# Performance work log

Hardware: AMD Instinct MI355X
Metric: run time of the kernel (lower is better)

## Reference

```python
import jax, jax.numpy as jnp
import numpy as np

N_NODES = 100000
N_EDGES = 1600000
F_IN, F_HID, N_CLS = 128, 128, 16


def setup_inputs() -> dict:
    key = jax.random.key(0)
    ks = jax.random.split(key, 6)
    x = jax.random.normal(ks[0], (N_NODES, F_IN), dtype=jnp.float32)
    edge_index = jax.random.randint(ks[1], (2, N_EDGES), 0, N_NODES, dtype=jnp.int64)
    # Glorot-ish scaled weights (PyG GCNConv uses glorot init, bias zeros)
    W1 = jax.random.normal(ks[2], (F_IN, F_HID), dtype=jnp.float32) * (1.0 / np.sqrt(F_IN))
    b1 = jnp.zeros((F_HID,), dtype=jnp.float32)
    W2 = jax.random.normal(ks[3], (F_HID, N_CLS), dtype=jnp.float32) * (1.0 / np.sqrt(F_HID))
    b2 = jnp.zeros((N_CLS,), dtype=jnp.float32)
    return {"x": x, "edge_index": edge_index, "W1": W1, "b1": b1, "W2": W2, "b2": b2}


def _gcn_conv(x, src, dst, W, b, num_nodes):
    """PyG GCNConv: y = D^{-1/2} (A + I) D^{-1/2} (x W) + b.
    src/dst already include self-loops."""
    h = x @ W  # [N, F_out]
    deg = jax.ops.segment_sum(jnp.ones_like(dst, dtype=h.dtype), dst, num_segments=num_nodes)
    dis = jnp.where(deg > 0, jax.lax.rsqrt(jnp.maximum(deg, 1e-12)), 0.0)
    norm = dis[src] * dis[dst]  # [E+N]
    msg = h[src] * norm[:, None]  # gather + scale  [E+N, F_out]
    out = jax.ops.segment_sum(msg, dst, num_segments=num_nodes)  # scatter-add at targets
    return out + b


def reference(x, edge_index, W1, b1, W2, b2):
    num_nodes = x.shape[0]
    loops = jnp.arange(num_nodes, dtype=edge_index.dtype)
    src = jnp.concatenate([edge_index[0], loops])
    dst = jnp.concatenate([edge_index[1], loops])
    h = _gcn_conv(x, src, dst, W1, b1, num_nodes)
    h = jax.nn.relu(h)
    # F.dropout with training=False (eval mode) is identity
    h = _gcn_conv(h, src, dst, W2, b2, num_nodes)
    return jax.nn.log_softmax(h, axis=1)
```

## Files before the change

### kernel.cpp

```cpp
#include <hip/hip_runtime.h>
#include <math.h>

#define N_NODES 100000
#define N_EDGES 1600000
#define NBINS 391
#define NCHUNK 400
#define CHUNK 4000
#define M_H (NBINS * NCHUNK)
#define NBLK_H 611

typedef __attribute__((ext_vector_type(8))) short bf16x8;
typedef __attribute__((ext_vector_type(4))) float f32x4;
typedef __attribute__((ext_vector_type(2))) float f32x2;

__device__ __forceinline__ unsigned short f2bf(float f) {
    unsigned int u = __float_as_uint(f);
    u += 0x7FFF + ((u >> 16) & 1);
    return (unsigned short)(u >> 16);
}
__device__ __forceinline__ float bf_lo(unsigned int u) { return __uint_as_float(u << 16); }
__device__ __forceinline__ float bf_hi(unsigned int u) { return __uint_as_float(u & 0xFFFF0000u); }
__device__ __forceinline__ f32x2 bfpair(unsigned int u) {
    f32x2 r; r.x = bf_lo(u); r.y = bf_hi(u); return r;
}


__global__ __launch_bounds__(256) void passA_kernel(const int* __restrict__ dst,
                                                    int* __restrict__ H) {
    __shared__ int lh[NBINS];
    int tid = threadIdx.x, c = blockIdx.x;
    for (int i = tid; i < NBINS; i += 256) lh[i] = 0;
    __syncthreads();
    int base = c * CHUNK;
    #pragma unroll
    for (int i = 0; i < 16; ++i) {
        int o = i * 256 + tid;
        if (o < CHUNK) atomicAdd(&lh[dst[base + o] >> 8], 1);
    }
    __syncthreads();
    for (int i = tid; i < NBINS; i += 256) H[i * NCHUNK + c] = lh[i];
}

__global__ __launch_bounds__(256) void scanB1_kernel(int* __restrict__ H,
                                                     int* __restrict__ blk2) {
    __shared__ int s[256];
    int t = threadIdx.x, i = blockIdx.x * 256 + t;
    int v = (i < M_H) ? H[i] : 0;
    s[t] = v;
    __syncthreads();
    for (int off = 1; off < 256; off <<= 1) {
        int u = (t >= off) ? s[t - off] : 0;
        __syncthreads();
        s[t] += u;
        __syncthreads();
    }
    if (i < M_H) H[i] = s[t] - v;
    if (t == 255) blk2[blockIdx.x] = s[255];
}

__global__ __launch_bounds__(1024) void scanB2_kernel(int* __restrict__ blk2) {
    __shared__ int s[1024];
    int t = threadIdx.x;
    int v = (t < NBLK_H) ? blk2[t] : 0;
    s[t] = v;
    __syncthreads();
    for (int off = 1; off < 1024; off <<= 1) {
        int u = (t >= off) ? s[t - off] : 0;
        __syncthreads();
        s[t] += u;
        __syncthreads();
    }
    if (t < NBLK_H) blk2[t] = s[t] - v;
}

__global__ __launch_bounds__(256) void passC_kernel(const int* __restrict__ src,
                                                    const int* __restrict__ dst,
                                                    const int* __restrict__ H,
                                                    const int* __restrict__ blk2,
                                                    int* __restrict__ rec,
                                                    const float* __restrict__ x,
                                                    const float* __restrict__ W1,
                                                    const float* __restrict__ W2,
                                                    ushort* __restrict__ xb,
                                                    ushort* __restrict__ W1T,
                                                    ushort* __restrict__ W2T) {
    int b = blockIdx.x;
    if (b < NCHUNK) {
        __shared__ int base[NBINS];
        __shared__ int rk[NBINS];
        int tid = threadIdx.x;
        for (int i = tid; i < NBINS; i += 256) {
            int idx = i * NCHUNK + b;
            base[i] = H[idx] + blk2[idx >> 8];
            rk[i] = 0;
        }
        __syncthreads();
        int estart = b * CHUNK;
        #pragma unroll
        for (int i = 0; i < 16; ++i) {
            int o = i * 256 + tid;
            if (o < CHUNK) {
                int e = estart + o;
                int d = dst[e];
                int bin = d >> 8;
                int r = atomicAdd(&rk[bin], 1);
                rec[base[bin] + r] = src[e] | ((d & 255) << 17);
            }
        }
    } else if (b < NCHUNK + 12500) {
        int i = (b - NCHUNK) * 256 + threadIdx.x;
        float4 v = *(const float4*)&x[i * 4];
        ushort4 o;
        o.x = f2bf(v.x); o.y = f2bf(v.y); o.z = f2bf(v.z); o.w = f2bf(v.w);
        *(ushort4*)&xb[i * 4] = o;
    } else {
        int j = (b - NCHUNK - 12500) * 256 + threadIdx.x;
        if (j < 16384) {
            int k = j >> 7, n = j & 127;
            W1T[n * 128 + k] = f2bf(W1[j]);
        } else {
            int q = j - 16384;
            int k = q >> 4, n = q & 15;
            W2T[n * 128 + k] = f2bf(W2[q]);
        }
    }
}

__global__ __launch_bounds__(256) void passD_kernel(const int* __restrict__ H,
                                                    const int* __restrict__ blk2,
                                                    const int* __restrict__ rec,
                                                    int* __restrict__ col,
                                                    int* __restrict__ cnt,
                                                    float* __restrict__ dis) {
    __shared__ int fh[256];
    __shared__ int s[256];
    __shared__ int run[256];
    int b = blockIdx.x, t = threadIdx.x;
    int i0 = b * NCHUNK;
    int estart = H[i0] + blk2[i0 >> 8];
    int eend;
    if (b == NBINS - 1) eend = N_EDGES;
    else { int i1 = (b + 1) * NCHUNK; eend = H[i1] + blk2[i1 >> 8]; }
    fh[t] = 0;
    __syncthreads();
    for (int e = estart + t; e < eend; e += 256)
        atomicAdd(&fh[rec[e] >> 17], 1);
    __syncthreads();
    int v = fh[t];
    s[t] = v;
    __syncthreads();
    for (int off = 1; off < 256; off <<= 1) {
        int u = (t >= off) ? s[t - off] : 0;
        __syncthreads();
        s[t] += u;
        __syncthreads();
    }
    int node = b * 256 + t;
    int start = estart + s[t] - v;
    run[t] = start;
    if (node < N_NODES) {
        cnt[node] = start;
        dis[node] = rsqrtf((float)v + 1.0f);
    }
    __syncthreads();
    for (int e = estart + t; e < eend; e += 256) {
        int r = rec[e];
        int p = atomicAdd(&run[r >> 17], 1);
        col[p] = r & 0x1FFFF;
    }
}


__global__ __launch_bounds__(256) void gather1_kernel(const int* __restrict__ col,
                                                      const int* __restrict__ cnt,
                                                      const float* __restrict__ dis,
                                                      const unsigned int* __restrict__ xb,
                                                      unsigned int* __restrict__ xa) {
    int t = threadIdx.x;
    int node = blockIdx.x * 4 + (t >> 6);
    int lane = t & 63;
    float dn = dis[node];
    int beg = cnt[node];
    int end = (node == N_NODES - 1) ? N_EDGES : cnt[node + 1];
    unsigned int su = xb[node * 64 + lane];
    f32x2 a0 = bfpair(su) * dn;
    f32x2 a1 = {0.f, 0.f}, a2 = {0.f, 0.f}, a3 = {0.f, 0.f};
    f32x2 a4 = {0.f, 0.f}, a5 = {0.f, 0.f}, a6 = {0.f, 0.f}, a7 = {0.f, 0.f};
    int k = beg;
    for (; k + 8 <= end; k += 8) {
        int s0 = col[k], s1 = col[k + 1], s2 = col[k + 2], s3 = col[k + 3];
        int s4 = col[k + 4], s5 = col[k + 5], s6 = col[k + 6], s7 = col[k + 7];
        float w0 = dis[s0], w1 = dis[s1], w2 = dis[s2], w3 = dis[s3];
        float w4 = dis[s4], w5 = dis[s5], w6 = dis[s6], w7 = dis[s7];
        unsigned int u0 = xb[s0 * 64 + lane], u1 = xb[s1 * 64 + lane];
        unsigned int u2 = xb[s2 * 64 + lane], u3 = xb[s3 * 64 + lane];
        unsigned int u4 = xb[s4 * 64 + lane], u5 = xb[s5 * 64 + lane];
        unsigned int u6 = xb[s6 * 64 + lane], u7 = xb[s7 * 64 + lane];
        a0 += bfpair(u0) * w0;
        a1 += bfpair(u1) * w1;
        a2 += bfpair(u2) * w2;
        a3 += bfpair(u3) * w3;
        a4 += bfpair(u4) * w4;
        a5 += bfpair(u5) * w5;
        a6 += bfpair(u6) * w6;
        a7 += bfpair(u7) * w7;
    }
    for (; k + 4 <= end; k += 4) {
        int s0 = col[k], s1 = col[k + 1], s2 = col[k + 2], s3 = col[k + 3];
        float w0 = dis[s0], w1 = dis[s1], w2 = dis[s2], w3 = dis[s3];
        unsigned int u0 = xb[s0 * 64 + lane], u1 = xb[s1 * 64 + lane];
        unsigned int u2 = xb[s2 * 64 + lane], u3 = xb[s3 * 64 + lane];
        a0 += bfpair(u0) * w0;
        a1 += bfpair(u1) * w1;
        a2 += bfpair(u2) * w2;
        a3 += bfpair(u3) * w3;
    }
    for (; k < end; ++k) {
        int s = col[k];
        float w = dis[s];
        a0 += bfpair(xb[s * 64 + lane]) * w;
    }
    f32x2 r = (((a0 + a1) + (a2 + a3)) + ((a4 + a5) + (a6 + a7))) * dn;
    xa[node * 64 + lane] = (unsigned int)f2bf(r.x) | ((unsigned int)f2bf(r.y) << 16);
}


__global__ __launch_bounds__(256) void mlp_kernel(const ushort* __restrict__ xa,
                                                  const ushort* __restrict__ W1T,
                                                  const float* __restrict__ b1,
                                                  const ushort* __restrict__ W2T,
                                                  ushort* __restrict__ h2b) {
    __shared__ ushort sh[4][16][136];
    int t = threadIdx.x;
    int wave = t >> 6, lane = t & 63;
    int l = lane & 15, quad = lane >> 4;
    int m0 = blockIdx.x * 64 + wave * 16;
    bool valid = (m0 < N_NODES);
    int row = valid ? (m0 + l) : 0;

    f32x4 acc[8] = {};
    #pragma unroll
    for (int kk = 0; kk < 4; ++kk) {
        bf16x8 a = *(const bf16x8*)&xa[row * 128 + kk * 32 + quad * 8];
        #pragma unroll
        for (int nt = 0; nt < 8; ++nt) {
            bf16x8 b = *(const bf16x8*)&W1T[(nt * 16 + l) * 128 + kk * 32 + quad * 8];
            acc[nt] = __builtin_amdgcn_mfma_f32_16x16x32_bf16(a, b, acc[nt], 0, 0, 0);
        }
    }
    #pragma unroll
    for (int nt = 0; nt < 8; ++nt) {
        float bias = b1[nt * 16 + l];
        #pragma unroll
        for (int r = 0; r < 4; ++r)
            sh[wave][quad * 4 + r][nt * 16 + l] = f2bf(fmaxf(acc[nt][r] + bias, 0.0f));
    }
    __syncthreads();

    f32x4 acc2 = {};
    #pragma unroll
    for (int kk = 0; kk < 4; ++kk) {
        bf16x8 a2 = *(const bf16x8*)&sh[wave][l][kk * 32 + quad * 8];
        bf16x8 bw = *(const bf16x8*)&W2T[l * 128 + kk * 32 + quad * 8];
        acc2 = __builtin_amdgcn_mfma_f32_16x16x32_bf16(a2, bw, acc2, 0, 0, 0);
    }
    if (valid) {
        #pragma unroll
        for (int r = 0; r < 4; ++r)
            h2b[(m0 + quad * 4 + r) * 16 + l] = f2bf(acc2[r]);
    }
}


__global__ __launch_bounds__(256) void gather2_lsm_kernel(const int* __restrict__ col,
                                                          const int* __restrict__ cnt,
                                                          const float* __restrict__ dis,
                                                          const unsigned int* __restrict__ h2p,
                                                          const float* __restrict__ b2,
                                                          float* __restrict__ out) {
    int t = threadIdx.x;
    int node = blockIdx.x * 32 + (t >> 3);
    int c = t & 7;
    float dn = dis[node];
    int beg = cnt[node];
    int end = (node == N_NODES - 1) ? N_EDGES : cnt[node + 1];
    unsigned int su = h2p[node * 8 + c];
    f32x2 a0 = bfpair(su) * dn;
    f32x2 a1 = {0.f, 0.f}, a2 = {0.f, 0.f}, a3 = {0.f, 0.f};
    f32x2 a4 = {0.f, 0.f}, a5 = {0.f, 0.f}, a6 = {0.f, 0.f}, a7 = {0.f, 0.f};
    int k = beg;
    for (; k + 8 <= end; k += 8) {
        int s0 = col[k], s1 = col[k + 1], s2 = col[k + 2], s3 = col[k + 3];
        int s4 = col[k + 4], s5 = col[k + 5], s6 = col[k + 6], s7 = col[k + 7];
        float w0 = dis[s0], w1 = dis[s1], w2 = dis[s2], w3 = dis[s3];
        float w4 = dis[s4], w5 = dis[s5], w6 = dis[s6], w7 = dis[s7];
        unsigned int u0 = h2p[s0 * 8 + c], u1 = h2p[s1 * 8 + c];
        unsigned int u2 = h2p[s2 * 8 + c], u3 = h2p[s3 * 8 + c];
        unsigned int u4 = h2p[s4 * 8 + c], u5 = h2p[s5 * 8 + c];
        unsigned int u6 = h2p[s6 * 8 + c], u7 = h2p[s7 * 8 + c];
        a0 += bfpair(u0) * w0;
        a1 += bfpair(u1) * w1;
        a2 += bfpair(u2) * w2;
        a3 += bfpair(u3) * w3;
        a4 += bfpair(u4) * w4;
        a5 += bfpair(u5) * w5;
        a6 += bfpair(u6) * w6;
        a7 += bfpair(u7) * w7;
    }
    for (; k + 4 <= end; k += 4) {
        int s0 = col[k], s1 = col[k + 1], s2 = col[k + 2], s3 = col[k + 3];
        float w0 = dis[s0], w1 = dis[s1], w2 = dis[s2], w3 = dis[s3];
        unsigned int u0 = h2p[s0 * 8 + c], u1 = h2p[s1 * 8 + c];
        unsigned int u2 = h2p[s2 * 8 + c], u3 = h2p[s3 * 8 + c];
        a0 += bfpair(u0) * w0;
        a1 += bfpair(u1) * w1;
        a2 += bfpair(u2) * w2;
        a3 += bfpair(u3) * w3;
    }
    for (; k < end; ++k) {
        int s = col[k];
        float w = dis[s];
        a0 += bfpair(h2p[s * 8 + c]) * w;
    }
    f32x2 r = ((a0 + a1) + (a2 + a3)) + ((a4 + a5) + (a6 + a7));
    float2 bb = ((const float2*)b2)[c];
    float v0 = r.x * dn + bb.x;
    float v1 = r.y * dn + bb.y;
    float m = fmaxf(v0, v1);
    #pragma unroll
    for (int off = 1; off < 8; off <<= 1) m = fmaxf(m, __shfl_xor(m, off, 8));
    float ssum = expf(v0 - m) + expf(v1 - m);
    #pragma unroll
    for (int off = 1; off < 8; off <<= 1) ssum += __shfl_xor(ssum, off, 8);
    float lg = m + logf(ssum);
    ((float2*)out)[node * 8 + c] = make_float2(v0 - lg, v1 - lg);
}


extern "C" void kernel_launch(void* const* d_in, const int* in_sizes, int n_in,
                              void* d_out, int out_size, void* d_ws, size_t ws_size,
                              hipStream_t stream) {
    const float* x  = (const float*)d_in[0];
    const int*   ei = (const int*)d_in[1];
    const float* W1 = (const float*)d_in[2];
    const float* b1 = (const float*)d_in[3];
    const float* W2 = (const float*)d_in[4];
    const float* b2 = (const float*)d_in[5];
    float* out = (float*)d_out;

    const int* src = ei;
    const int* dst = ei + N_EDGES;

    char* ws = (char*)d_ws;
    ushort* xb   = (ushort*)(ws + 0);
    ushort* h2b  = (ushort*)(ws + 0);
    ushort* xa   = (ushort*)(ws + 25600000);
    int*    rec  = (int*)   (ws + 25600000);
    int*    H    = (int*)   (ws + 32000000);
    int*    col  = (int*)   (ws + 51200000);
    float*  dis  = (float*) (ws + 57600000);
    int*    cnt  = (int*)   (ws + 58000000);
    int*    blk2 = (int*)   (ws + 58400000);
    ushort* W1T  = (ushort*)(ws + 58404096);
    ushort* W2T  = (ushort*)(ws + 58436864);

    passA_kernel      <<<NCHUNK, 256, 0, stream>>>(dst, H);
    scanB1_kernel     <<<NBLK_H, 256, 0, stream>>>(H, blk2);
    scanB2_kernel     <<<1, 1024, 0, stream>>>(blk2);
    passC_kernel      <<<NCHUNK + 12500 + 72, 256, 0, stream>>>(src, dst, H, blk2, rec,
                                                                x, W1, W2, xb, W1T, W2T);
    passD_kernel      <<<NBINS, 256, 0, stream>>>(H, blk2, rec, col, cnt, dis);

    gather1_kernel    <<<N_NODES / 4, 256, 0, stream>>>(col, cnt, dis,
                                                        (const unsigned int*)xb,
                                                        (unsigned int*)xa);
    mlp_kernel        <<<1563, 256, 0, stream>>>(xa, W1T, b1, W2T, h2b);
    gather2_lsm_kernel<<<3125, 256, 0, stream>>>(col, cnt, dis,
                                                 (const unsigned int*)h2b, b2, out);
}
```

Baseline: 272.7 us.

## Fuse first-layer neighbor gather into the MLP kernel via shared memory

Merges the layer-1 aggregation kernel into the MLP kernel. Each wave gathers 16 nodes sequentially into a shared-memory tile, and the MFMA matmuls then read that tile instead of a global intermediate. This removes the global write and re-read of the aggregated feature buffer and one kernel launch. The workspace layout changes so h2b no longer aliases xb. The cost is fewer, larger blocks with more LDS per block. That likely lowers resident waves and memory-level parallelism for the latency-bound gather, and adds serial per-wave node loops with tail imbalance.

```diff
diff --git a/kernel.cpp b/kernel.cpp
--- a/kernel.cpp
+++ b/kernel.cpp
@@ -171,77 +171,77 @@
 }
 
 
-__global__ __launch_bounds__(256) void gather1_kernel(const int* __restrict__ col,
-                                                      const int* __restrict__ cnt,
-                                                      const float* __restrict__ dis,
-                                                      const unsigned int* __restrict__ xb,
-                                                      unsigned int* __restrict__ xa) {
-    int t = threadIdx.x;
-    int node = blockIdx.x * 4 + (t >> 6);
-    int lane = t & 63;
-    float dn = dis[node];
-    int beg = cnt[node];
-    int end = (node == N_NODES - 1) ? N_EDGES : cnt[node + 1];
-    unsigned int su = xb[node * 64 + lane];
-    f32x2 a0 = bfpair(su) * dn;
-    f32x2 a1 = {0.f, 0.f}, a2 = {0.f, 0.f}, a3 = {0.f, 0.f};
-    f32x2 a4 = {0.f, 0.f}, a5 = {0.f, 0.f}, a6 = {0.f, 0.f}, a7 = {0.f, 0.f};
-    int k = beg;
-    for (; k + 8 <= end; k += 8) {
-        int s0 = col[k], s1 = col[k + 1], s2 = col[k + 2], s3 = col[k + 3];
-        int s4 = col[k + 4], s5 = col[k + 5], s6 = col[k + 6], s7 = col[k + 7];
-        float w0 = dis[s0], w1 = dis[s1], w2 = dis[s2], w3 = dis[s3];
-        float w4 = dis[s4], w5 = dis[s5], w6 = dis[s6], w7 = dis[s7];
-        unsigned int u0 = xb[s0 * 64 + lane], u1 = xb[s1 * 64 + lane];
-        unsigned int u2 = xb[s2 * 64 + lane], u3 = xb[s3 * 64 + lane];
-        unsigned int u4 = xb[s4 * 64 + lane], u5 = xb[s5 * 64 + lane];
-        unsigned int u6 = xb[s6 * 64 + lane], u7 = xb[s7 * 64 + lane];
-        a0 += bfpair(u0) * w0;
-        a1 += bfpair(u1) * w1;
-        a2 += bfpair(u2) * w2;
-        a3 += bfpair(u3) * w3;
-        a4 += bfpair(u4) * w4;
-        a5 += bfpair(u5) * w5;
-        a6 += bfpair(u6) * w6;
-        a7 += bfpair(u7) * w7;
-    }
-    for (; k + 4 <= end; k += 4) {
-        int s0 = col[k], s1 = col[k + 1], s2 = col[k + 2], s3 = col[k + 3];
-        float w0 = dis[s0], w1 = dis[s1], w2 = dis[s2], w3 = dis[s3];
-        unsigned int u0 = xb[s0 * 64 + lane], u1 = xb[s1 * 64 + lane];
-        unsigned int u2 = xb[s2 * 64 + lane], u3 = xb[s3 * 64 + lane];
-        a0 += bfpair(u0) * w0;
-        a1 += bfpair(u1) * w1;
-        a2 += bfpair(u2) * w2;
-        a3 += bfpair(u3) * w3;
-    }
-    for (; k < end; ++k) {
-        int s = col[k];
-        float w = dis[s];
-        a0 += bfpair(xb[s * 64 + lane]) * w;
-    }
-    f32x2 r = (((a0 + a1) + (a2 + a3)) + ((a4 + a5) + (a6 + a7))) * dn;
-    xa[node * 64 + lane] = (unsigned int)f2bf(r.x) | ((unsigned int)f2bf(r.y) << 16);
-}
-
-
-__global__ __launch_bounds__(256) void mlp_kernel(const ushort* __restrict__ xa,
-                                                  const ushort* __restrict__ W1T,
-                                                  const float* __restrict__ b1,
-                                                  const ushort* __restrict__ W2T,
-                                                  ushort* __restrict__ h2b) {
-    __shared__ ushort sh[4][16][136];
+__global__ __launch_bounds__(256) void gather_mlp_kernel(const int* __restrict__ col,
+                                                         const int* __restrict__ cnt,
+                                                         const float* __restrict__ dis,
+                                                         const unsigned int* __restrict__ xb,
+                                                         const ushort* __restrict__ W1T,
+                                                         const float* __restrict__ b1,
+                                                         const ushort* __restrict__ W2T,
+                                                         ushort* __restrict__ h2b) {
+    __shared__ ushort shx[64][136];
+    __shared__ ushort shh[4][16][136];
     int t = threadIdx.x;
     int wave = t >> 6, lane = t & 63;
     int l = lane & 15, quad = lane >> 4;
-    int m0 = blockIdx.x * 64 + wave * 16;
-    bool valid = (m0 < N_NODES);
-    int row = valid ? (m0 + l) : 0;
+    int m0 = blockIdx.x * 64;
+
+    for (int i = 0; i < 16; ++i) {
+        int node = m0 + wave * 16 + i;
+        unsigned int packed = 0;
+        if (node < N_NODES) {
+            float dn = dis[node];
+            int beg = cnt[node];
+            int end = (node == N_NODES - 1) ? N_EDGES : cnt[node + 1];
+            unsigned int su = xb[node * 64 + lane];
+            f32x2 a0 = bfpair(su) * dn;
+            f32x2 a1 = {0.f, 0.f}, a2 = {0.f, 0.f}, a3 = {0.f, 0.f};
+            f32x2 a4 = {0.f, 0.f}, a5 = {0.f, 0.f}, a6 = {0.f, 0.f}, a7 = {0.f, 0.f};
+            int k = beg;
+            for (; k + 8 <= end; k += 8) {
+                int s0 = col[k], s1 = col[k + 1], s2 = col[k + 2], s3 = col[k + 3];
+                int s4 = col[k + 4], s5 = col[k + 5], s6 = col[k + 6], s7 = col[k + 7];
+                float w0 = dis[s0], w1 = dis[s1], w2 = dis[s2], w3 = dis[s3];
+                float w4 = dis[s4], w5 = dis[s5], w6 = dis[s6], w7 = dis[s7];
+                unsigned int u0 = xb[s0 * 64 + lane], u1 = xb[s1 * 64 + lane];
+                unsigned int u2 = xb[s2 * 64 + lane], u3 = xb[s3 * 64 + lane];
+                unsigned int u4 = xb[s4 * 64 + lane], u5 = xb[s5 * 64 + lane];
+                unsigned int u6 = xb[s6 * 64 + lane], u7 = xb[s7 * 64 + lane];
+                a0 += bfpair(u0) * w0;
+                a1 += bfpair(u1) * w1;
+                a2 += bfpair(u2) * w2;
+                a3 += bfpair(u3) * w3;
+                a4 += bfpair(u4) * w4;
+                a5 += bfpair(u5) * w5;
+                a6 += bfpair(u6) * w6;
+                a7 += bfpair(u7) * w7;
+            }
+            for (; k + 4 <= end; k += 4) {
+                int s0 = col[k], s1 = col[k + 1], s2 = col[k + 2], s3 = col[k + 3];
+                float w0 = dis[s0], w1 = dis[s1], w2 = dis[s2], w3 = dis[s3];
+                unsigned int u0 = xb[s0 * 64 + lane], u1 = xb[s1 * 64 + lane];
+                unsigned int u2 = xb[s2 * 64 + lane], u3 = xb[s3 * 64 + lane];
+                a0 += bfpair(u0) * w0;
+                a1 += bfpair(u1) * w1;
+                a2 += bfpair(u2) * w2;
+                a3 += bfpair(u3) * w3;
+            }
+            for (; k < end; ++k) {
+                int s = col[k];
+                float w = dis[s];
+                a0 += bfpair(xb[s * 64 + lane]) * w;
+            }
+            f32x2 r = (((a0 + a1) + (a2 + a3)) + ((a4 + a5) + (a6 + a7))) * dn;
+            packed = (unsigned int)f2bf(r.x) | ((unsigned int)f2bf(r.y) << 16);
+        }
+        *(unsigned int*)&shx[wave * 16 + i][lane * 2] = packed;
+    }
+    __syncthreads();
 
     f32x4 acc[8] = {};
     #pragma unroll
     for (int kk = 0; kk < 4; ++kk) {
-        bf16x8 a = *(const bf16x8*)&xa[row * 128 + kk * 32 + quad * 8];
+        bf16x8 a = *(const bf16x8*)&shx[wave * 16 + l][kk * 32 + quad * 8];
         #pragma unroll
         for (int nt = 0; nt < 8; ++nt) {
             bf16x8 b = *(const bf16x8*)&W1T[(nt * 16 + l) * 128 + kk * 32 + quad * 8];
@@ -253,21 +253,22 @@
         float bias = b1[nt * 16 + l];
         #pragma unroll
         for (int r = 0; r < 4; ++r)
-            sh[wave][quad * 4 + r][nt * 16 + l] = f2bf(fmaxf(acc[nt][r] + bias, 0.0f));
+            shh[wave][quad * 4 + r][nt * 16 + l] = f2bf(fmaxf(acc[nt][r] + bias, 0.0f));
     }
     __syncthreads();
 
     f32x4 acc2 = {};
     #pragma unroll
     for (int kk = 0; kk < 4; ++kk) {
-        bf16x8 a2 = *(const bf16x8*)&sh[wave][l][kk * 32 + quad * 8];
+        bf16x8 a2 = *(const bf16x8*)&shh[wave][l][kk * 32 + quad * 8];
         bf16x8 bw = *(const bf16x8*)&W2T[l * 128 + kk * 32 + quad * 8];
         acc2 = __builtin_amdgcn_mfma_f32_16x16x32_bf16(a2, bw, acc2, 0, 0, 0);
     }
-    if (valid) {
-        #pragma unroll
-        for (int r = 0; r < 4; ++r)
-            h2b[(m0 + quad * 4 + r) * 16 + l] = f2bf(acc2[r]);
+    int mw = m0 + wave * 16;
+    #pragma unroll
+    for (int r = 0; r < 4; ++r) {
+        int m = mw + quad * 4 + r;
+        if (m < N_NODES) h2b[m * 16 + l] = f2bf(acc2[r]);
     }
 }
 
@@ -353,10 +354,9 @@
 
     char* ws = (char*)d_ws;
     ushort* xb   = (ushort*)(ws + 0);
-    ushort* h2b  = (ushort*)(ws + 0);
-    ushort* xa   = (ushort*)(ws + 25600000);
-    int*    rec  = (int*)   (ws + 25600000);
-    int*    H    = (int*)   (ws + 32000000);
+    ushort* h2b  = (ushort*)(ws + 25600000);
+    int*    rec  = (int*)   (ws + 28800000);
+    int*    H    = (int*)   (ws + 35200000);
     int*    col  = (int*)   (ws + 51200000);
     float*  dis  = (float*) (ws + 57600000);
     int*    cnt  = (int*)   (ws + 58000000);
@@ -371,10 +371,9 @@
                                                                 x, W1, W2, xb, W1T, W2T);
     passD_kernel      <<<NBINS, 256, 0, stream>>>(H, blk2, rec, col, cnt, dis);
 
-    gather1_kernel    <<<N_NODES / 4, 256, 0, stream>>>(col, cnt, dis,
-                                                        (const unsigned int*)xb,
-                                                        (unsigned int*)xa);
-    mlp_kernel        <<<1563, 256, 0, stream>>>(xa, W1T, b1, W2T, h2b);
+    gather_mlp_kernel <<<1563, 256, 0, stream>>>(col, cnt, dis,
+                                                 (const unsigned int*)xb,
+                                                 W1T, b1, W2T, h2b);
     gather2_lsm_kernel<<<3125, 256, 0, stream>>>(col, cnt, dis,
                                                  (const unsigned int*)h2b, b2, out);
 }
```

After: 297.6 us. +9.1%, slower.
